# Optimization experiments

Hardware: AMD Instinct MI355X
Metric: run time of the kernel (lower is better)

The kernel has to match this reference:

```python
import jax, jax.numpy as jnp
import numpy as np

AC_KERNEL = 5


def deconv(x, w, stride):
    """torch ConvTranspose2d(k=3, p=1, bias=False), stride 1 or 2 (output_padding=1).
    w has torch layout [Cin, Cout, kH, kW]."""
    wk = jnp.transpose(w, (1, 0, 2, 3))[:, :, ::-1, ::-1]  # OIHW, spatially flipped
    dn = ('NCHW', 'OIHW', 'NCHW')
    if stride == 1:
        return jax.lax.conv_general_dilated(x, wk, (1, 1), ((1, 1), (1, 1)), dimension_numbers=dn)
    # stride 2: dilate input, pad (k-1-p, k-1-p+op) = (1, 2) -> doubles H, W
    return jax.lax.conv_general_dilated(x, wk, (1, 1), ((1, 2), (1, 2)),
                                        lhs_dilation=(2, 2), dimension_numbers=dn)


def sepconv(feat, kv, kh, K):
    """Per-pixel adaptive separable convolution (Niklaus SepConv).
    feat: [B,C,H,W]; kv, kh: [B,K,H,W]. Replication-pad by K//2, then
    out[b,c,y,x] = sum_{i,j} pad[b,c,y+i,x+j] * kv[b,i,y,x] * kh[b,j,y,x]."""
    pad = K // 2
    B, C, H, W = feat.shape
    p = jnp.pad(feat, ((0, 0), (0, 0), (pad, pad), (pad, pad)), mode='edge')
    out = jnp.zeros_like(feat)
    for i in range(K):  # small fixed loop over kernel taps
        row = p[:, :, i:i + H, :]  # [B,C,H,W+2*pad]
        horiz = row[:, :, :, 0:W] * kh[:, 0:1]
        for j in range(1, K):
            horiz = horiz + row[:, :, :, j:j + W] * kh[:, j:j + 1]
        out = out + kv[:, i:i + 1] * horiz
    return out


def fusion(feat, kv, kh, mask):
    tmp = sepconv(feat, kv, kh, AC_KERNEL)
    return mask * tmp + (1.0 - mask) * feat


def setup_inputs() -> dict:
    key = jax.random.key(0)
    ks = jax.random.split(key, 20)
    B, G = 128, 64
    d = {'cont_feat': jax.random.normal(ks[0], (B, G, 8, 8), jnp.float32)}
    sizes = [8, 16, 32, 64]
    for li, s in enumerate(sizes):
        d[f'kv{li}'] = jax.random.uniform(ks[1 + 3 * li], (B, AC_KERNEL, s, s), jnp.float32)
        d[f'kh{li}'] = jax.random.uniform(ks[2 + 3 * li], (B, AC_KERNEL, s, s), jnp.float32)
        d[f'm{li}'] = jax.random.uniform(ks[3 + 3 * li], (B, 1, s, s), jnp.float32)
    wshapes = [(G, G * 8, 3, 3), (G * 8, G * 4, 3, 3), (G * 4, G * 2, 3, 3),
               (G * 2, G * 2, 3, 3), (G * 2, G, 3, 3), (G, 3, 3, 3)]
    for wi, ws in enumerate(wshapes):
        d[f'w{wi + 1}'] = jax.random.normal(ks[13 + wi], ws, jnp.float32) * 0.05
    return d


def reference(cont_feat, kv0, kh0, m0, kv1, kh1, m1, kv2, kh2, m2, kv3, kh3, m3,
              w1, w2, w3, w4, w5, w6):
    # kernel_layer = 4, no_mask = False, use_bn = False
    feat_8 = fusion(cont_feat, kv0, kh0, m0)                      # [B,G,8,8]
    feat_16 = jax.nn.relu(deconv(feat_8, w1, 2))                  # [B,8G,16,16]
    feat_16 = fusion(feat_16, kv1, kh1, m1)
    h = jax.nn.relu(deconv(feat_16, w2, 1))                       # [B,4G,16,16]
    feat_32 = jax.nn.relu(deconv(h, w3, 2))                       # [B,2G,32,32]
    feat_32 = fusion(feat_32, kv2, kh2, m2)
    h = jax.nn.relu(deconv(feat_32, w4, 1))                       # [B,2G,32,32]
    h = jax.nn.relu(deconv(h, w5, 2))                             # [B,G,64,64]
    out = jnp.tanh(deconv(h, w6, 1))                              # [B,3,64,64]
    out = fusion(out, kv3, kh3, m3)
    return (out, feat_8, feat_16, feat_32)
```

## Files before the change

kernel.cpp:

```cpp
#include <hip/hip_runtime.h>
#include <math.h>

typedef short v8s __attribute__((ext_vector_type(8)));
typedef float v16f __attribute__((ext_vector_type(16)));

__device__ inline unsigned short f2bf(float f) {
    union { float f; unsigned u; } c; c.f = f;
    unsigned r = (c.u + 0x7fffu + ((c.u >> 16) & 1u)) >> 16;
    return (unsigned short)r;
}

template<int LW>
__global__ __launch_bounds__(256) void fusion2_kernel(
        const float* __restrict__ feat, const float* __restrict__ kv,
        const float* __restrict__ kh, const float* __restrict__ m,
        float* __restrict__ out, int C, int CH, int H, int lhw) {
    constexpr int W = 1 << LW;
    const int t = blockIdx.x * 256 + threadIdx.x;
    const int hw = H << LW;
    const int b = t >> lhw;
    const int pix = t & (hw - 1);
    const int x = pix & (W - 1);
    const int y = pix >> LW;
    const int lane = threadIdx.x & 63;
    const int rowbase = (lane & ~(W - 1)) << 2;

    const int c0 = blockIdx.y * CH;

    const float mv = m[(size_t)b * hw + pix];
    float kvv[5], khv[5];
#pragma unroll
    for (int i = 0; i < 5; i++) {
        kvv[i] = kv[((size_t)b * 5 + i) * hw + pix];
        khv[i] = kh[((size_t)b * 5 + i) * hw + pix];
    }
    int idx[5];
#pragma unroll
    for (int j = 0; j < 5; j++) {
        int xx = x + j - 2; xx = xx < 0 ? 0 : (xx >= W ? W - 1 : xx);
        idx[j] = rowbase + (xx << 2);
    }
    int roff[5];
#pragma unroll
    for (int i = 0; i < 5; i++) {
        int yy = y + i - 2; yy = yy < 0 ? 0 : (yy >= H ? H - 1 : yy);
        roff[i] = (yy << LW) + x;
    }

    const float* fbase = feat + ((size_t)b * C + c0) * hw;
    float* obase = out + ((size_t)b * C + c0) * hw + pix;
    const float om = 1.f - mv;

#pragma unroll 4
    for (int cc = 0; cc < CH; cc++) {
        const float* q = fbase + (size_t)cc * hw;
        float s = 0.f;
        float fv = 0.f;
#pragma unroll
        for (int i = 0; i < 5; i++) {
            float v = q[roff[i]];
            if (i == 2) fv = v;
            int vb = __float_as_int(v);
            float h = 0.f;
#pragma unroll
            for (int j = 0; j < 5; j++) {
                float nv = __int_as_float(
                    __builtin_amdgcn_ds_bpermute(idx[j], vb));
                h += nv * khv[j];
            }
            s += kvv[i] * h;
        }
        obase[(size_t)cc * hw] = mv * s + om * fv;
    }
}

__global__ __launch_bounds__(256) void nchw_to_nhwc_bf16(
        const float* __restrict__ in, unsigned short* __restrict__ out,
        int C, int H, int W, int lw, int lc2) {
    extern __shared__ unsigned short sm_t[];
    const int y = blockIdx.x, b = blockIdx.y;
    const int Cp = C + 8;
    const int tid = threadIdx.x;
    for (int i = tid; i < C * W; i += 256) {
        int x = i & (W - 1), c = i >> lw;
        float v = in[(((size_t)b * C + c) * H + y) * W + x];
        sm_t[x * Cp + c] = f2bf(v);
    }
    __syncthreads();
    const unsigned* s32 = (const unsigned*)sm_t;
    unsigned* o32 = (unsigned*)(out + (((size_t)b * H + y) * W) * C);
    const int n32 = (W * C) >> 1;
    for (int i = tid; i < n32; i += 256) {
        int x = i >> lc2;
        int c2 = i - (x << lc2);
        o32[i] = s32[x * (Cp >> 1) + c2];
    }
}

__global__ __launch_bounds__(256) void repack_w_frag(
        const float* __restrict__ w, unsigned short* __restrict__ wk,
        int Cin, int Cout, int flip) {
    int idx = blockIdx.x * 256 + threadIdx.x;
    if (idx >= Cin * Cout) return;
    int ci = idx / Cout, co = idx - ci * Cout;
    const float* src = w + (size_t)idx * 9;
    const int nCb = Cout >> 5, nH = Cin >> 4;
    const size_t inner = (size_t)((((ci >> 3) & 1) * 32 + (co & 31)) * 8 + (ci & 7));
#pragma unroll
    for (int k = 0; k < 9; k++) {
        int t = flip ? (8 - k) : k;
        size_t blk = ((size_t)t * nCb + (co >> 5)) * nH + (ci >> 4);
        wk[(blk << 9) + inner] = f2bf(src[k]);
    }
}

template<int W, int TH, int LW>
__global__ __launch_bounds__(256) void conv3x3_mfma(
        const unsigned short* __restrict__ X,
        const unsigned short* __restrict__ Wk,
        unsigned short* __restrict__ out, int Cin, int Cout, int H) {
    constexpr int TP = (TH + 2) * (W + 2);
    constexpr int NIT = TP * 4;
    constexpr int NLD = (NIT + 255) / 256;
    __shared__ unsigned short sB[2][TP * 40];
    const int tid = threadIdx.x;
    const int lane = tid & 63, wv = tid >> 6;
    const int wm = wv >> 1, wn = wv & 1;
    const int y0 = blockIdx.x * TH;
    const int coB = blockIdx.y * 128 + wm * 64;
    const int b = blockIdx.z;
    const int n = lane & 31, kg = lane >> 5;
    const int p0 = wn * 64 + n, p1 = p0 + 32;
    const int r0 = p0 >> LW, c0 = p0 & (W - 1);
    const int r1 = p1 >> LW, c1 = p1 & (W - 1);
    const int bo0 = (r0 * (W + 2) + c0) * 40 + kg * 8;
    const int bo1 = (r1 * (W + 2) + c1) * 40 + kg * 8;
    v16f acc00 = {}, acc01 = {}, acc10 = {}, acc11 = {};
    const size_t cbStride = (size_t)(Cin >> 4) << 9;
    const size_t tStride  = (size_t)(Cout >> 5) * cbStride;
    const unsigned short* Af = Wk + (size_t)(coB >> 5) * cbStride + (lane << 3);
    const unsigned short* Xb = X + (size_t)b * H * W * Cin;

    const unsigned short* ldp[NLD];
    int sto[NLD];
#pragma unroll
    for (int s = 0; s < NLD; s++) {
        int i = tid + s * 256;
        bool slot = (i < NIT);
        int pix = i >> 2, part = i & 3;
        int py = pix / (W + 2), px = pix - py * (W + 2);
        int gy = y0 + py - 1, gx = px - 1;
        bool ok = slot && gy >= 0 && gy < H && (unsigned)gx < (unsigned)W;
        ldp[s] = ok ? Xb + ((size_t)(gy * W + gx)) * Cin + part * 8 : nullptr;
        sto[s] = slot ? pix * 40 + part * 8 : -1;
    }

    uint4 pre[NLD];
#pragma unroll
    for (int s = 0; s < NLD; s++)
        pre[s] = ldp[s] ? *(const uint4*)(ldp[s]) : make_uint4(0u, 0u, 0u, 0u);
#pragma unroll
    for (int s = 0; s < NLD; s++)
        if (sto[s] >= 0) *(uint4*)(sB[0] + sto[s]) = pre[s];
    __syncthreads();

    const int NK = Cin >> 5;
    for (int kk = 0; kk < NK; kk++) {
        const int cur = kk & 1;
        const int ci0 = kk << 5;
        const bool more = (kk + 1 < NK);
        if (more) {
#pragma unroll
            for (int s = 0; s < NLD; s++)
                pre[s] = ldp[s] ? *(const uint4*)(ldp[s] + ci0 + 32)
                                : make_uint4(0u, 0u, 0u, 0u);
        }
        const unsigned short* sC = sB[cur];
#pragma unroll
        for (int t = 0; t < 9; t++) {
            const int ky = t / 3, kx = t - ky * 3;
            const int toff = (ky * (W + 2) + kx) * 40;
#pragma unroll
            for (int kh = 0; kh < 2; kh++) {
                const unsigned short* ap =
                    Af + (size_t)t * tStride + (size_t)(((ci0 >> 4) + kh) << 9);
                v8s A0 = *(const v8s*)(ap);
                v8s A1 = *(const v8s*)(ap + cbStride);
                v8s B0 = *(const v8s*)(sC + bo0 + toff + kh * 16);
                v8s B1 = *(const v8s*)(sC + bo1 + toff + kh * 16);
                acc00 = __builtin_amdgcn_mfma_f32_32x32x16_bf16(A0, B0, acc00, 0, 0, 0);
                acc01 = __builtin_amdgcn_mfma_f32_32x32x16_bf16(A0, B1, acc01, 0, 0, 0);
                acc10 = __builtin_amdgcn_mfma_f32_32x32x16_bf16(A1, B0, acc10, 0, 0, 0);
                acc11 = __builtin_amdgcn_mfma_f32_32x32x16_bf16(A1, B1, acc11, 0, 0, 0);
            }
        }
        if (more) {
            unsigned short* sN = sB[cur ^ 1];
#pragma unroll
            for (int s = 0; s < NLD; s++)
                if (sto[s] >= 0) *(uint4*)(sN + sto[s]) = pre[s];
            __syncthreads();
        }
    }
    unsigned short* ob = out + (size_t)b * H * W * Cout;
#pragma unroll
    for (int sm = 0; sm < 2; sm++) {
        v16f a0 = sm ? acc10 : acc00;
        v16f a1 = sm ? acc11 : acc01;
        const int cobase = coB + sm * 32 + 4 * kg;
        unsigned short* q0p = ob + ((size_t)((y0 + r0) * W + c0)) * Cout + cobase;
        unsigned short* q1p = ob + ((size_t)((y0 + r1) * W + c1)) * Cout + cobase;
#pragma unroll
        for (int r2 = 0; r2 < 4; r2++) {
            ushort4 q0, q1; float v;
            v = a0[4 * r2 + 0]; v = v > 0.f ? v : 0.f; q0.x = f2bf(v);
            v = a0[4 * r2 + 1]; v = v > 0.f ? v : 0.f; q0.y = f2bf(v);
            v = a0[4 * r2 + 2]; v = v > 0.f ? v : 0.f; q0.z = f2bf(v);
            v = a0[4 * r2 + 3]; v = v > 0.f ? v : 0.f; q0.w = f2bf(v);
            *(ushort4*)(q0p + 8 * r2) = q0;
            v = a1[4 * r2 + 0]; v = v > 0.f ? v : 0.f; q1.x = f2bf(v);
            v = a1[4 * r2 + 1]; v = v > 0.f ? v : 0.f; q1.y = f2bf(v);
            v = a1[4 * r2 + 2]; v = v > 0.f ? v : 0.f; q1.z = f2bf(v);
            v = a1[4 * r2 + 3]; v = v > 0.f ? v : 0.f; q1.w = f2bf(v);
            *(ushort4*)(q1p + 8 * r2) = q1;
        }
    }
}

template<int W, int TH, int NWN, int NWM, int LW>
__global__ __launch_bounds__(256) void deconv2_mfma(
        const unsigned short* __restrict__ X,
        const unsigned short* __restrict__ Wk,
        float* __restrict__ out, int Cin, int Cout, int Hin) {
    constexpr int ROWS = NWN * TH + 1;
    constexpr int NPIX = ROWS * (W + 1);
    constexpr int NIT = NPIX * 4;
    constexpr int NLD = (NIT + 255) / 256;
    __shared__ unsigned short sB[2][NPIX * 40];
    const int tid = threadIdx.x;
    const int lane = tid & 63, wv = tid >> 6;
    const int wm = wv / NWN, wn = wv % NWN;
    const int n = lane & 31, kg = lane >> 5;
    const int y0 = blockIdx.x * (NWN * TH);
    const int coB = (blockIdx.y * NWM + wm) * 64;
    const int b = blockIdx.z;
    const int Yl = wn * TH + (n >> LW);
    const int Xl = n & (W - 1);
    v16f zero = {};
    v16f acc[2][2][2];
#pragma unroll
    for (int i = 0; i < 2; i++)
#pragma unroll
        for (int j = 0; j < 2; j++)
#pragma unroll
            for (int s = 0; s < 2; s++) acc[i][j][s] = zero;
    const unsigned short* Xb = X + (size_t)b * Hin * W * Cin;
    const size_t cbStride = (size_t)(Cin >> 4) << 9;
    const size_t tStride  = (size_t)(Cout >> 5) * cbStride;
    const unsigned short* Af = Wk + (size_t)(coB >> 5) * cbStride + (lane << 3);
    const int PY[3] = {1, 0, 1}, DY[3] = {1, 0, 0};

    const unsigned short* ldp[NLD];
    int sto[NLD];
#pragma unroll
    for (int s = 0; s < NLD; s++) {
        int i = tid + s * 256;
        bool slot = (i < NIT);
        int pix = i >> 2, part = i & 3;
        int py_ = pix / (W + 1), px_ = pix - py_ * (W + 1);
        int gy = y0 + py_, gx = px_;
        bool ok = slot && gy < Hin && gx < W;
        ldp[s] = ok ? Xb + ((size_t)(gy * W + gx)) * Cin + part * 8 : nullptr;
        sto[s] = slot ? pix * 40 + part * 8 : -1;
    }

    uint4 pre[NLD];
#pragma unroll
    for (int s = 0; s < NLD; s++)
        pre[s] = ldp[s] ? *(const uint4*)(ldp[s]) : make_uint4(0u, 0u, 0u, 0u);
#pragma unroll
    for (int s = 0; s < NLD; s++)
        if (sto[s] >= 0) *(uint4*)(sB[0] + sto[s]) = pre[s];
    __syncthreads();

    const int NK = Cin >> 5;
    for (int kk = 0; kk < NK; kk++) {
        const int cur = kk & 1;
        const int ci0 = kk << 5;
        const bool more = (kk + 1 < NK);
        if (more) {
#pragma unroll
            for (int s = 0; s < NLD; s++)
                pre[s] = ldp[s] ? *(const uint4*)(ldp[s] + ci0 + 32)
                                : make_uint4(0u, 0u, 0u, 0u);
        }
        const unsigned short* sC = sB[cur];
#pragma unroll
        for (int ky = 0; ky < 3; ky++) {
#pragma unroll
            for (int kx = 0; kx < 3; kx++) {
                const int py = PY[ky], dy = DY[ky];
                const int px = PY[kx], dx = DY[kx];
                const int t = ky * 3 + kx;
                const int boff = ((Yl + dy) * (W + 1) + (Xl + dx)) * 40 + kg * 8;
#pragma unroll
                for (int kh = 0; kh < 2; kh++) {
                    const unsigned short* ap =
                        Af + (size_t)t * tStride + (size_t)(((ci0 >> 4) + kh) << 9);
                    v8s B  = *(const v8s*)(sC + boff + kh * 16);
                    v8s A0 = *(const v8s*)(ap);
                    v8s A1 = *(const v8s*)(ap + cbStride);
                    acc[py][px][0] = __builtin_amdgcn_mfma_f32_32x32x16_bf16(A0, B, acc[py][px][0], 0, 0, 0);
                    acc[py][px][1] = __builtin_amdgcn_mfma_f32_32x32x16_bf16(A1, B, acc[py][px][1], 0, 0, 0);
                }
            }
        }
        if (more) {
            unsigned short* sN = sB[cur ^ 1];
#pragma unroll
            for (int s = 0; s < NLD; s++)
                if (sto[s] >= 0) *(uint4*)(sN + sto[s]) = pre[s];
            __syncthreads();
        }
    }
    const int Wo = 2 * W, Ho = 2 * Hin;
    const int yin = y0 + Yl;
#pragma unroll
    for (int py = 0; py < 2; py++) {
        const int oy = 2 * yin + py;
#pragma unroll
        for (int sm = 0; sm < 2; sm++) {
            const int cobase = coB + sm * 32 + 4 * kg;
#pragma unroll
            for (int r = 0; r < 16; r++) {
                int co = cobase + (r & 3) + 8 * (r >> 2);
                float v0 = acc[py][0][sm][r]; v0 = v0 > 0.f ? v0 : 0.f;
                float v1 = acc[py][1][sm][r]; v1 = v1 > 0.f ? v1 : 0.f;
                *(float2*)(out + (((size_t)(b * Cout + co) * Ho + oy) * Wo + 2 * Xl)) =
                    make_float2(v0, v1);
            }
        }
    }
}

__global__ __launch_bounds__(256) void conv_s1_c3_tanh_kernel(
        const float* __restrict__ in, const float* __restrict__ w,
        float* __restrict__ out, int Cin, int H, int W) {
    __shared__ float sIn[8][18][19];
    __shared__ float sW[8][3][9];
    const int tid = threadIdx.x;
    const int r = tid >> 4, c = tid & 15;
    const int ntx = W >> 4;
    const int tx0 = (blockIdx.x % ntx) << 4, ty0 = (blockIdx.x / ntx) << 4;
    const int b = blockIdx.z;
    const int hw = H * W;
    float acc[3] = {0.f, 0.f, 0.f};
    for (int ci0 = 0; ci0 < Cin; ci0 += 8) {
        for (int i = tid; i < 8 * 18 * 18; i += 256) {
            int ci = i / 324, rr = i % 324, ly = rr / 18, lx = rr % 18;
            int gy = ty0 + ly - 1, gx = tx0 + lx - 1;
            float v = 0.f;
            if (gy >= 0 && gy < H && gx >= 0 && gx < W)
                v = in[(size_t)(b * Cin + ci0 + ci) * hw + gy * W + gx];
            sIn[ci][ly][lx] = v;
        }
        for (int i = tid; i < 8 * 3 * 9; i += 256) {
            int ci = i / 27, rr = i % 27, co = rr / 9, k = rr % 9;
            sW[ci][co][k] = w[(size_t)((ci0 + ci) * 3 + co) * 9 + (8 - k)];
        }
        __syncthreads();
#pragma unroll
        for (int ci = 0; ci < 8; ci++) {
            float v00 = sIn[ci][r][c],     v01 = sIn[ci][r][c + 1],     v02 = sIn[ci][r][c + 2];
            float v10 = sIn[ci][r + 1][c], v11 = sIn[ci][r + 1][c + 1], v12 = sIn[ci][r + 1][c + 2];
            float v20 = sIn[ci][r + 2][c], v21 = sIn[ci][r + 2][c + 1], v22 = sIn[ci][r + 2][c + 2];
#pragma unroll
            for (int co = 0; co < 3; co++) {
                const float* wp = &sW[ci][co][0];
                acc[co] += v00 * wp[0] + v01 * wp[1] + v02 * wp[2]
                         + v10 * wp[3] + v11 * wp[4] + v12 * wp[5]
                         + v20 * wp[6] + v21 * wp[7] + v22 * wp[8];
            }
        }
        __syncthreads();
    }
#pragma unroll
    for (int co = 0; co < 3; co++)
        out[(size_t)(b * 3 + co) * hw + (ty0 + r) * W + tx0 + c] = tanhf(acc[co]);
}

extern "C" void kernel_launch(void* const* d_in, const int* in_sizes, int n_in,
                              void* d_out, int out_size, void* d_ws, size_t ws_size,
                              hipStream_t stream) {
    const float* cont = (const float*)d_in[0];
    const float* kv0 = (const float*)d_in[1];
    const float* kh0 = (const float*)d_in[2];
    const float* m0  = (const float*)d_in[3];
    const float* kv1 = (const float*)d_in[4];
    const float* kh1 = (const float*)d_in[5];
    const float* m1  = (const float*)d_in[6];
    const float* kv2 = (const float*)d_in[7];
    const float* kh2 = (const float*)d_in[8];
    const float* m2  = (const float*)d_in[9];
    const float* kv3 = (const float*)d_in[10];
    const float* kh3 = (const float*)d_in[11];
    const float* m3  = (const float*)d_in[12];
    const float* w1  = (const float*)d_in[13];
    const float* w2  = (const float*)d_in[14];
    const float* w3  = (const float*)d_in[15];
    const float* w4  = (const float*)d_in[16];
    const float* w5  = (const float*)d_in[17];
    const float* w6  = (const float*)d_in[18];

    float* out = (float*)d_out;
    float* f8  = out + 1572864;
    float* f16 = out + 2097152;
    float* f32 = out + 18874368;

    char* ws = (char*)d_ws;

    float* A0 = (float*)ws;
    unsigned short* X8  = (unsigned short*)(ws + 67108864);
    unsigned short* Wk1 = (unsigned short*)(ws + 68157440);

    fusion2_kernel<3><<<dim3(32, 4), 256, 0, stream>>>(
        cont, kv0, kh0, m0, f8, 64, 16, 8, 6);
    nchw_to_nhwc_bf16<<<dim3(8, 128), 256, 8 * 72 * 2, stream>>>(f8, X8, 64, 8, 8, 3, 5);
    repack_w_frag<<<128, 256, 0, stream>>>(w1, Wk1, 64, 512, 0);
    deconv2_mfma<8, 4, 2, 2, 3><<<dim3(1, 4, 128), 256, 0, stream>>>(
        X8, Wk1, A0, 64, 512, 8);
    fusion2_kernel<4><<<dim3(128, 32), 256, 0, stream>>>(
        A0, kv1, kh1, m1, f16, 512, 16, 16, 8);

    unsigned short* X16 = (unsigned short*)ws;
    unsigned short* h1b = (unsigned short*)(ws + 67108864);
    unsigned short* Wk3 = (unsigned short*)(ws + 83886080);
    unsigned short* Wk2 = (unsigned short*)(ws + 84475904);
    nchw_to_nhwc_bf16<<<dim3(16, 128), 256, 16 * 520 * 2, stream>>>(
        f16, X16, 512, 16, 16, 4, 8);
    repack_w_frag<<<512, 256, 0, stream>>>(w2, Wk2, 512, 256, 1);
    conv3x3_mfma<16, 8, 4><<<dim3(2, 2, 128), 256, 0, stream>>>(
        X16, Wk2, h1b, 512, 256, 16);
    repack_w_frag<<<128, 256, 0, stream>>>(w3, Wk3, 256, 128, 0);
    float* t32 = (float*)ws;
    deconv2_mfma<16, 2, 2, 2, 4><<<dim3(4, 1, 128), 256, 0, stream>>>(
        h1b, Wk3, t32, 256, 128, 16);
    fusion2_kernel<5><<<dim3(512, 8), 256, 0, stream>>>(
        t32, kv2, kh2, m2, f32, 128, 16, 32, 10);

    unsigned short* Wk4  = (unsigned short*)ws;
    unsigned short* Wk5  = (unsigned short*)(ws + 294912);
    unsigned short* X32q = (unsigned short*)(ws + 524288);
    unsigned short* h2b  = (unsigned short*)(ws + 8912896);
    float* h3q = (float*)(ws + 17301504);
    float* tq  = (float*)(ws + 50855936);
    repack_w_frag<<<64, 256, 0, stream>>>(w4, Wk4, 128, 128, 1);
    repack_w_frag<<<32, 256, 0, stream>>>(w5, Wk5, 128, 64, 0);
    for (int q = 0; q < 4; q++) {
        size_t bo = (size_t)q * 32;
        const float* f32q = f32 + bo * 128 * 1024;
        nchw_to_nhwc_bf16<<<dim3(32, 32), 256, 32 * 136 * 2, stream>>>(
            f32q, X32q, 128, 32, 32, 5, 6);
        conv3x3_mfma<32, 4, 5><<<dim3(8, 1, 32), 256, 0, stream>>>(
            X32q, Wk4, h2b, 128, 128, 32);
        deconv2_mfma<32, 1, 4, 1, 5><<<dim3(8, 1, 32), 256, 0, stream>>>(
            h2b, Wk5, h3q, 128, 64, 32);
        conv_s1_c3_tanh_kernel<<<dim3(16, 1, 32), 256, 0, stream>>>(h3q, w6, tq, 64, 64, 64);
        fusion2_kernel<6><<<dim3(512, 1), 256, 0, stream>>>(
            tq, kv3 + bo * 5 * 4096, kh3 + bo * 5 * 4096, m3 + bo * 4096,
            out + bo * 3 * 4096, 3, 3, 64, 12);
    }
}
```

Before: 1.045 ms.

## Software-pipeline MFMA operand loads and batch 32x32 conv across full batch

Restructures the inner MFMA loops of the conv3x3 and stride-2 deconv kernels so A fragments are prefetched three steps ahead and B fragments one step ahead in rotating register buffers. This hides global and LDS load latency behind the matrix ops. When the workspace is large enough, it also runs the NHWC conversion and the 32x32 conv over all 128 images in one launch instead of four quarter-batch launches. That gives larger grids and fewer launches, at the cost of more workspace and more live registers.

```diff
diff --git a/kernel.cpp b/kernel.cpp
--- a/kernel.cpp
+++ b/kernel.cpp
@@ -176,24 +176,38 @@
                                 : make_uint4(0u, 0u, 0u, 0u);
         }
         const unsigned short* sC = sB[cur];
-#pragma unroll
-        for (int t = 0; t < 9; t++) {
+        const unsigned short* Abase2 = Af + ((size_t)(ci0 >> 4) << 9);
+
+        auto ldA = [&](int s, v8s &a0, v8s &a1) {
+            const int t = s >> 1, kh = s & 1;
+            const unsigned short* ap = Abase2 + (size_t)t * tStride + (kh << 9);
+            a0 = *(const v8s*)(ap);
+            a1 = *(const v8s*)(ap + cbStride);
+        };
+        auto ldB = [&](int s, v8s &b0v, v8s &b1v) {
+            const int t = s >> 1, kh = s & 1;
             const int ky = t / 3, kx = t - ky * 3;
-            const int toff = (ky * (W + 2) + kx) * 40;
-#pragma unroll
-            for (int kh = 0; kh < 2; kh++) {
-                const unsigned short* ap =
-                    Af + (size_t)t * tStride + (size_t)(((ci0 >> 4) + kh) << 9);
-                v8s A0 = *(const v8s*)(ap);
-                v8s A1 = *(const v8s*)(ap + cbStride);
-                v8s B0 = *(const v8s*)(sC + bo0 + toff + kh * 16);
-                v8s B1 = *(const v8s*)(sC + bo1 + toff + kh * 16);
-                acc00 = __builtin_amdgcn_mfma_f32_32x32x16_bf16(A0, B0, acc00, 0, 0, 0);
-                acc01 = __builtin_amdgcn_mfma_f32_32x32x16_bf16(A0, B1, acc01, 0, 0, 0);
-                acc10 = __builtin_amdgcn_mfma_f32_32x32x16_bf16(A1, B0, acc10, 0, 0, 0);
-                acc11 = __builtin_amdgcn_mfma_f32_32x32x16_bf16(A1, B1, acc11, 0, 0, 0);
-            }
-        }
+            const int off = (ky * (W + 2) + kx) * 40 + kh * 16;
+            b0v = *(const v8s*)(sC + bo0 + off);
+            b1v = *(const v8s*)(sC + bo1 + off);
+        };
+
+        v8s A0p[3], A1p[3], B0p[2], B1p[2];
+        ldA(0, A0p[0], A1p[0]);
+        ldA(1, A0p[1], A1p[1]);
+        ldA(2, A0p[2], A1p[2]);
+        ldB(0, B0p[0], B1p[0]);
+#pragma unroll
+        for (int s = 0; s < 18; s++) {
+            const int ca = s % 3, cb = s & 1;
+            if (s + 1 < 18) ldB(s + 1, B0p[cb ^ 1], B1p[cb ^ 1]);
+            acc00 = __builtin_amdgcn_mfma_f32_32x32x16_bf16(A0p[ca], B0p[cb], acc00, 0, 0, 0);
+            acc01 = __builtin_amdgcn_mfma_f32_32x32x16_bf16(A0p[ca], B1p[cb], acc01, 0, 0, 0);
+            acc10 = __builtin_amdgcn_mfma_f32_32x32x16_bf16(A1p[ca], B0p[cb], acc10, 0, 0, 0);
+            acc11 = __builtin_amdgcn_mfma_f32_32x32x16_bf16(A1p[ca], B1p[cb], acc11, 0, 0, 0);
+            if (s + 3 < 18) ldA(s + 3, A0p[ca], A1p[ca]);
+        }
+
         if (more) {
             unsigned short* sN = sB[cur ^ 1];
 #pragma unroll
@@ -295,26 +309,39 @@
                                 : make_uint4(0u, 0u, 0u, 0u);
         }
         const unsigned short* sC = sB[cur];
-#pragma unroll
-        for (int ky = 0; ky < 3; ky++) {
-#pragma unroll
-            for (int kx = 0; kx < 3; kx++) {
-                const int py = PY[ky], dy = DY[ky];
-                const int px = PY[kx], dx = DY[kx];
-                const int t = ky * 3 + kx;
-                const int boff = ((Yl + dy) * (W + 1) + (Xl + dx)) * 40 + kg * 8;
-#pragma unroll
-                for (int kh = 0; kh < 2; kh++) {
-                    const unsigned short* ap =
-                        Af + (size_t)t * tStride + (size_t)(((ci0 >> 4) + kh) << 9);
-                    v8s B  = *(const v8s*)(sC + boff + kh * 16);
-                    v8s A0 = *(const v8s*)(ap);
-                    v8s A1 = *(const v8s*)(ap + cbStride);
-                    acc[py][px][0] = __builtin_amdgcn_mfma_f32_32x32x16_bf16(A0, B, acc[py][px][0], 0, 0, 0);
-                    acc[py][px][1] = __builtin_amdgcn_mfma_f32_32x32x16_bf16(A1, B, acc[py][px][1], 0, 0, 0);
-                }
-            }
-        }
+        const unsigned short* Abase2 = Af + ((size_t)(ci0 >> 4) << 9);
+
+        auto ldA = [&](int s, v8s &a0, v8s &a1) {
+            const int t = s >> 1, kh = s & 1;
+            const unsigned short* ap = Abase2 + (size_t)t * tStride + (kh << 9);
+            a0 = *(const v8s*)(ap);
+            a1 = *(const v8s*)(ap + cbStride);
+        };
+        auto ldB = [&](int s, v8s &bv) {
+            const int t = s >> 1, kh = s & 1;
+            const int ky = t / 3, kx = t - ky * 3;
+            const int boff = ((Yl + DY[ky]) * (W + 1) + (Xl + DY[kx])) * 40
+                             + kg * 8 + kh * 16;
+            bv = *(const v8s*)(sC + boff);
+        };
+
+        v8s A0p[3], A1p[3], Bp[2];
+        ldA(0, A0p[0], A1p[0]);
+        ldA(1, A0p[1], A1p[1]);
+        ldA(2, A0p[2], A1p[2]);
+        ldB(0, Bp[0]);
+#pragma unroll
+        for (int s = 0; s < 18; s++) {
+            const int ca = s % 3, cb = s & 1;
+            if (s + 1 < 18) ldB(s + 1, Bp[cb ^ 1]);
+            const int t = s >> 1;
+            const int ky = t / 3, kx = t - ky * 3;
+            const int py = PY[ky], px = PY[kx];
+            acc[py][px][0] = __builtin_amdgcn_mfma_f32_32x32x16_bf16(A0p[ca], Bp[cb], acc[py][px][0], 0, 0, 0);
+            acc[py][px][1] = __builtin_amdgcn_mfma_f32_32x32x16_bf16(A1p[ca], Bp[cb], acc[py][px][1], 0, 0, 0);
+            if (s + 3 < 18) ldA(s + 3, A0p[ca], A1p[ca]);
+        }
+
         if (more) {
             unsigned short* sN = sB[cur ^ 1];
 #pragma unroll
@@ -448,26 +475,50 @@
     fusion2_kernel<5><<<dim3(512, 8), 256, 0, stream>>>(
         t32, kv2, kh2, m2, f32, 128, 16, 32, 10);
 
-    unsigned short* Wk4  = (unsigned short*)ws;
-    unsigned short* Wk5  = (unsigned short*)(ws + 294912);
-    unsigned short* X32q = (unsigned short*)(ws + 524288);
-    unsigned short* h2b  = (unsigned short*)(ws + 8912896);
-    float* h3q = (float*)(ws + 17301504);
-    float* tq  = (float*)(ws + 50855936);
-    repack_w_frag<<<64, 256, 0, stream>>>(w4, Wk4, 128, 128, 1);
-    repack_w_frag<<<32, 256, 0, stream>>>(w5, Wk5, 128, 64, 0);
-    for (int q = 0; q < 4; q++) {
-        size_t bo = (size_t)q * 32;
-        const float* f32q = f32 + bo * 128 * 1024;
-        nchw_to_nhwc_bf16<<<dim3(32, 32), 256, 32 * 136 * 2, stream>>>(
-            f32q, X32q, 128, 32, 32, 5, 6);
-        conv3x3_mfma<32, 4, 5><<<dim3(8, 1, 32), 256, 0, stream>>>(
-            X32q, Wk4, h2b, 128, 128, 32);
-        deconv2_mfma<32, 1, 4, 1, 5><<<dim3(8, 1, 32), 256, 0, stream>>>(
-            h2b, Wk5, h3q, 128, 64, 32);
-        conv_s1_c3_tanh_kernel<<<dim3(16, 1, 32), 256, 0, stream>>>(h3q, w6, tq, 64, 64, 64);
-        fusion2_kernel<6><<<dim3(512, 1), 256, 0, stream>>>(
-            tq, kv3 + bo * 5 * 4096, kh3 + bo * 5 * 4096, m3 + bo * 4096,
-            out + bo * 3 * 4096, 3, 3, 64, 12);
-    }
-}
+    if (ws_size >= (size_t)102760448) {
+        unsigned short* Wk4 = (unsigned short*)ws;
+        unsigned short* Wk5 = (unsigned short*)(ws + 294912);
+        unsigned short* X32 = (unsigned short*)(ws + 524288);
+        unsigned short* h2b = (unsigned short*)(ws + 34078720);
+        float* h3q = (float*)(ws + 67633152);
+        float* tq  = (float*)(ws + 101187584);
+        repack_w_frag<<<64, 256, 0, stream>>>(w4, Wk4, 128, 128, 1);
+        repack_w_frag<<<32, 256, 0, stream>>>(w5, Wk5, 128, 64, 0);
+        nchw_to_nhwc_bf16<<<dim3(32, 128), 256, 32 * 136 * 2, stream>>>(
+            f32, X32, 128, 32, 32, 5, 6);
+        conv3x3_mfma<32, 4, 5><<<dim3(8, 1, 128), 256, 0, stream>>>(
+            X32, Wk4, h2b, 128, 128, 32);
+        for (int q = 0; q < 4; q++) {
+            size_t bo = (size_t)q * 32;
+            deconv2_mfma<32, 1, 4, 1, 5><<<dim3(8, 1, 32), 256, 0, stream>>>(
+                h2b + bo * 131072, Wk5, h3q, 128, 64, 32);
+            conv_s1_c3_tanh_kernel<<<dim3(16, 1, 32), 256, 0, stream>>>(h3q, w6, tq, 64, 64, 64);
+            fusion2_kernel<6><<<dim3(512, 1), 256, 0, stream>>>(
+                tq, kv3 + bo * 5 * 4096, kh3 + bo * 5 * 4096, m3 + bo * 4096,
+                out + bo * 3 * 4096, 3, 3, 64, 12);
+        }
+    } else {
+        unsigned short* Wk4  = (unsigned short*)ws;
+        unsigned short* Wk5  = (unsigned short*)(ws + 294912);
+        unsigned short* X32q = (unsigned short*)(ws + 524288);
+        unsigned short* h2b  = (unsigned short*)(ws + 8912896);
+        float* h3q = (float*)(ws + 17301504);
+        float* tq  = (float*)(ws + 50855936);
+        repack_w_frag<<<64, 256, 0, stream>>>(w4, Wk4, 128, 128, 1);
+        repack_w_frag<<<32, 256, 0, stream>>>(w5, Wk5, 128, 64, 0);
+        for (int q = 0; q < 4; q++) {
+            size_t bo = (size_t)q * 32;
+            const float* f32q = f32 + bo * 128 * 1024;
+            nchw_to_nhwc_bf16<<<dim3(32, 32), 256, 32 * 136 * 2, stream>>>(
+                f32q, X32q, 128, 32, 32, 5, 6);
+            conv3x3_mfma<32, 4, 5><<<dim3(8, 1, 32), 256, 0, stream>>>(
+                X32q, Wk4, h2b, 128, 128, 32);
+            deconv2_mfma<32, 1, 4, 1, 5><<<dim3(8, 1, 32), 256, 0, stream>>>(
+                h2b, Wk5, h3q, 128, 64, 32);
+            conv_s1_c3_tanh_kernel<<<dim3(16, 1, 32), 256, 0, stream>>>(h3q, w6, tq, 64, 64, 64);
+            fusion2_kernel<6><<<dim3(512, 1), 256, 0, stream>>>(
+                tq, kv3 + bo * 5 * 4096, kh3 + bo * 5 * 4096, m3 + bo * 4096,
+                out + bo * 3 * 4096, 3, 3, 64, 12);
+        }
+    }
+}
```

New measurement: 984.3 us. 1.06x faster.
